# Performance work log

Measured on AMD Instinct MI355X. Metric: run time of the kernel, lower is better.

The kernel has to match this reference:

```python
import jax, jax.numpy as jnp
import numpy as np

B, D, C, Q = 4096, 128, 1000, 65536
PROTO_M = 0.99
EPS = 1e-12


def _l2norm(x, axis=-1):
    n = jnp.sqrt(jnp.sum(x * x, axis=axis, keepdims=True))
    return x / jnp.maximum(n, EPS)


def setup_inputs() -> dict:
    key = jax.random.key(0)
    ks = jax.random.split(key, 7)
    q = _l2norm(jax.random.normal(ks[0], (B, D), dtype=jnp.float32))
    k = _l2norm(jax.random.normal(ks[1], (B, D), dtype=jnp.float32))
    classfy_logits = jax.random.normal(ks[2], (B, C), dtype=jnp.float32)
    plabel = jax.random.uniform(ks[3], (B, C), dtype=jnp.float32)
    prototypes = _l2norm(jax.random.normal(ks[4], (C, D), dtype=jnp.float32))
    queue = _l2norm(jax.random.normal(ks[5], (Q, D), dtype=jnp.float32))
    queue_pseudo = jax.random.randint(ks[6], (Q,), 0, C).astype(jnp.float32)
    return {
        "q": q, "k": k, "classfy_logits": classfy_logits, "plabel": plabel,
        "prototypes": prototypes, "queue": queue, "queue_pseudo": queue_pseudo,
        "ptr": 0,
    }


def reference(q, k, classfy_logits, plabel, prototypes, queue, queue_pseudo, ptr):
    m = PROTO_M
    # classifier softmax (encoder head output)
    classfy_out = jax.nn.softmax(classfy_logits, axis=1)          # [B, C]
    # cluster logits against OLD prototypes (mm happens before EMA update)
    logits_prot = jnp.matmul(q, prototypes.T)                     # [B, C]
    cluster_out = jax.nn.softmax(logits_prot, axis=1)
    # pseudo labels from partial-label-masked scores
    pseudo_labels = jnp.argmax(classfy_out * plabel, axis=1)      # [B] int
    # --- vectorized order-dependent scatter-EMA prototype update ---
    # sequential: proto[l_i] = m*proto[l_i] + (1-m)*q_i  for i = 0..B-1
    # closed form: proto[c]*m^{n_c} + sum_i (1-m)*m^{(#later samples with same label)} q_i
    onehot = (pseudo_labels[:, None] == jnp.arange(C)[None, :])   # [B, C] bool
    counts = jnp.sum(onehot, axis=0)                              # [C] n_c
    rank = jnp.take_along_axis(jnp.cumsum(onehot.astype(jnp.int32), axis=0),
                               pseudo_labels[:, None], axis=1)[:, 0] - 1  # [B]
    n_l = counts[pseudo_labels]                                   # [B]
    w = (1.0 - m) * jnp.power(jnp.float32(m), (n_l - 1 - rank).astype(jnp.float32))
    scatter = jnp.zeros_like(prototypes).at[pseudo_labels].add(w[:, None] * q)
    decay = jnp.power(jnp.float32(m), counts.astype(jnp.float32))[:, None]
    new_prototypes = _l2norm(prototypes * decay + scatter, axis=1)
    # --- MoCo queue enqueue/dequeue (contrastive bank uses OLD queue) ---
    cont_features = jnp.concatenate([q, k, queue], axis=0)        # [2B+Q, D]
    pl_f = pseudo_labels.astype(jnp.float32)
    cont_labels = jnp.concatenate([pl_f, pl_f, queue_pseudo], axis=0)
    new_queue = jax.lax.dynamic_update_slice(queue, k, (ptr, 0))
    new_queue_pseudo = jax.lax.dynamic_update_slice(queue_pseudo, pl_f, (ptr,))
    new_ptr = (ptr + q.shape[0]) % queue.shape[0]
    return (classfy_out, cluster_out, cont_features, cont_labels,
            new_prototypes, new_queue, new_queue_pseudo, new_ptr)
```

## Files before the change

kernel.cpp:

```cpp
#include <hip/hip_runtime.h>
#include <hip/hip_bf16.h>
#include <math.h>

#define Bn 4096
#define Dn 128
#define Cn 1000
#define Qn 65536

typedef __attribute__((ext_vector_type(8))) short short8v;
typedef __attribute__((ext_vector_type(4))) short short4v;
typedef __attribute__((ext_vector_type(4))) float f32x4;
typedef __attribute__((ext_vector_type(4))) float f4v;

__device__ inline float waveAllMaxF(float v) {
    for (int o = 32; o; o >>= 1) v = fmaxf(v, __shfl_xor(v, o));
    return v;
}
__device__ inline float waveAllSumF(float v) {
    for (int o = 32; o; o >>= 1) v += __shfl_xor(v, o);
    return v;
}
__device__ inline float waveSumF(float v) {
    for (int o = 32; o; o >>= 1) v += __shfl_down(v, o);
    return v;
}
__device__ inline short f2bf(float x) {
    union { __hip_bfloat16 h; short s; } u;
    u.h = __float2bfloat16(x);
    return u.s;
}

__global__ __launch_bounds__(256) void k_cls(
    const float* __restrict__ logits, const float* __restrict__ plabel,
    const float* __restrict__ q, const float* __restrict__ proto,
    float* __restrict__ out_cls, int* __restrict__ labels,
    __hip_bfloat16* __restrict__ qb, __hip_bfloat16* __restrict__ pb)
{
    int g = blockIdx.x, t = threadIdx.x;

    if (t < 160) {
        int idx4 = g * 160 + t;
        if (idx4 < 131072) {
            f4v v = *(const f4v*)(q + (long long)idx4 * 4);
            short4v o = {f2bf(v.x), f2bf(v.y), f2bf(v.z), f2bf(v.w)};
            *(short4v*)((short*)qb + (long long)idx4 * 4) = o;
        } else {
            int j4 = idx4 - 131072;
            short4v o = {0, 0, 0, 0};
            if (j4 < 32000) {
                f4v v = *(const f4v*)(proto + (long long)j4 * 4);
                o = (short4v){f2bf(v.x), f2bf(v.y), f2bf(v.z), f2bf(v.w)};
            }
            *(short4v*)((short*)pb + (long long)j4 * 4) = o;
        }
    }

    int lane = t & 63, wid = t >> 6;
    int row = g * 4 + wid;
    const float* x  = logits + (long long)row * Cn;
    const float* pl = plabel + (long long)row * Cn;

    f4v lv[4], pv[4];
#pragma unroll
    for (int j = 0; j < 4; ++j) {
        int f4i = lane + j * 64;
        if (f4i < 250) {
            lv[j] = *(const f4v*)(x + f4i * 4);
            pv[j] = *(const f4v*)(pl + f4i * 4);
        } else {
            lv[j] = (f4v){-INFINITY, -INFINITY, -INFINITY, -INFINITY};
            pv[j] = (f4v){0.f, 0.f, 0.f, 0.f};
        }
    }

    float mx = -INFINITY;
#pragma unroll
    for (int j = 0; j < 4; ++j)
        mx = fmaxf(mx, fmaxf(fmaxf(lv[j].x, lv[j].y), fmaxf(lv[j].z, lv[j].w)));
    mx = waveAllMaxF(mx);

    float vv[16];
    float ssum = 0.f;
#pragma unroll
    for (int j = 0; j < 4; ++j) {
        vv[j * 4 + 0] = expf(lv[j].x - mx);
        vv[j * 4 + 1] = expf(lv[j].y - mx);
        vv[j * 4 + 2] = expf(lv[j].z - mx);
        vv[j * 4 + 3] = expf(lv[j].w - mx);
        ssum += vv[j * 4 + 0] + vv[j * 4 + 1] + vv[j * 4 + 2] + vv[j * 4 + 3];
    }
    ssum = waveAllSumF(ssum);
    float inv = 1.f / ssum;

    float bv = -INFINITY; int bi = Cn;
#pragma unroll
    for (int j = 0; j < 4; ++j) {
        int f4i = lane + j * 64;
        if (f4i < 250) {
            float o0 = vv[j * 4 + 0] * inv, o1 = vv[j * 4 + 1] * inv;
            float o2 = vv[j * 4 + 2] * inv, o3 = vv[j * 4 + 3] * inv;
            *((f4v*)(out_cls + (long long)row * Cn) + f4i) = (f4v){o0, o1, o2, o3};
            float pr[4] = {o0 * pv[j].x, o1 * pv[j].y, o2 * pv[j].z, o3 * pv[j].w};
#pragma unroll
            for (int jj = 0; jj < 4; ++jj) {
                if (pr[jj] > bv) { bv = pr[jj]; bi = f4i * 4 + jj; }
            }
        }
    }
    for (int o = 32; o; o >>= 1) {
        float ov = __shfl_xor(bv, o);
        int   oi = __shfl_xor(bi, o);
        if (ov > bv || (ov == bv && oi < bi)) { bv = ov; bi = oi; }
    }
    if (lane == 0) labels[row] = bi;
}

__global__ __launch_bounds__(256) void k_rest(
    const __hip_bfloat16* __restrict__ qb, const __hip_bfloat16* __restrict__ pbuf,
    const float* __restrict__ proto, const float* __restrict__ q,
    const float* __restrict__ kk, const float* __restrict__ queue,
    const int* __restrict__ lbl, const float* __restrict__ qps,
    const int* __restrict__ ptrp,
    float* __restrict__ outC, float* __restrict__ outp,
    float* __restrict__ out_lab, float* __restrict__ out_qps,
    float* __restrict__ out_ptr,
    float* __restrict__ out_feat, float* __restrict__ out_queue)
{
    __shared__ __align__(16) char smem[32800];
    int bid = blockIdx.x, t = threadIdx.x;

    if (bid < 256) {
        float (*red)[4] = (float (*)[4])smem;
        int lane = t & 63, w = t >> 6;
        int la = lane & 15, lk = lane >> 4;
        int row0 = bid * 16;

        f32x4 acc[16];
#pragma unroll
        for (int j = 0; j < 16; ++j) acc[j] = (f32x4){0.f, 0.f, 0.f, 0.f};

        const short* A = (const short*)qb + (long long)(row0 + la) * Dn;
        const short* Bp = (const short*)pbuf;
#pragma unroll
        for (int kc = 0; kc < Dn; kc += 32) {
            short8v a = *(const short8v*)(A + kc + lk * 8);
#pragma unroll
            for (int j = 0; j < 16; ++j) {
                int prow = w * 256 + j * 16 + la;
                short8v b = *(const short8v*)(Bp + (long long)prow * Dn + kc + lk * 8);
                acc[j] = __builtin_amdgcn_mfma_f32_16x16x32_bf16(a, b, acc[j], 0, 0, 0);
            }
        }

        float m[4];
#pragma unroll
        for (int rg = 0; rg < 4; ++rg) {
            float v = -INFINITY;
#pragma unroll
            for (int j = 0; j < 16; ++j) {
                int col = w * 256 + j * 16 + la;
                if (col < Cn) v = fmaxf(v, acc[j][rg]);
            }
#pragma unroll
            for (int o = 1; o < 16; o <<= 1) v = fmaxf(v, __shfl_xor(v, o));
            m[rg] = v;
        }
        if (la == 0) {
#pragma unroll
            for (int rg = 0; rg < 4; ++rg) red[lk * 4 + rg][w] = m[rg];
        }
        __syncthreads();
#pragma unroll
        for (int rg = 0; rg < 4; ++rg) {
            int r = lk * 4 + rg;
            m[rg] = fmaxf(fmaxf(red[r][0], red[r][1]), fmaxf(red[r][2], red[r][3]));
        }
        __syncthreads();

        float s[4];
#pragma unroll
        for (int rg = 0; rg < 4; ++rg) {
            float v = 0.f;
#pragma unroll
            for (int j = 0; j < 16; ++j) {
                int col = w * 256 + j * 16 + la;
                float e = (col < Cn) ? expf(acc[j][rg] - m[rg]) : 0.f;
                acc[j][rg] = e;
                v += e;
            }
#pragma unroll
            for (int o = 1; o < 16; o <<= 1) v += __shfl_xor(v, o);
            s[rg] = v;
        }
        if (la == 0) {
#pragma unroll
            for (int rg = 0; rg < 4; ++rg) red[lk * 4 + rg][w] = s[rg];
        }
        __syncthreads();
#pragma unroll
        for (int rg = 0; rg < 4; ++rg) {
            int r = lk * 4 + rg;
            s[rg] = 1.f / (red[r][0] + red[r][1] + red[r][2] + red[r][3]);
        }

#pragma unroll
        for (int j = 0; j < 16; ++j) {
            int col = w * 256 + j * 16 + la;
            if (col < Cn) {
                int rowb = row0 + lk * 4;
#pragma unroll
                for (int rg = 0; rg < 4; ++rg)
                    outC[(long long)(rowb + rg) * Cn + col] = acc[j][rg] * s[rg];
            }
        }
    } else if (bid < 756) {
        int* sl = (int*)smem;
        unsigned short* list0 = (unsigned short*)(smem + 16384);
        unsigned short* list1 = list0 + 4096;
        int* nm = (int*)(smem + 32768);
        float* shh = (float*)(smem + 32776);

        int h = t >> 7, tt = t & 127;
        int c = (bid - 256) * 2 + h;

#pragma unroll
        for (int u = 0; u < 4; ++u) {
            int base = (u * 256 + t) * 4;
            *(int4*)(sl + base) = *(const int4*)(lbl + base);
        }
        if (t == 0)   nm[0] = 0;
        if (t == 128) nm[1] = 0;
        __syncthreads();

        int wv = t >> 6;
        if ((wv & 1) == 0) {
            int hh = wv >> 1;
            int ln = t & 63;
            int cc = (bid - 256) * 2 + hh;
            unsigned short* lst = hh ? list1 : list0;
            int n = 0;
            for (int jj = 0; jj < Bn / 64; ++jj) {
                unsigned long long mask = __ballot(sl[jj * 64 + ln] == cc);
                if (ln == 0) {
                    while (mask) {
                        int b = __builtin_ctzll(mask);
                        lst[n++] = (unsigned short)(jj * 64 + b);
                        mask &= mask - 1;
                    }
                }
            }
            if (ln == 0) nm[hh] = n;
        }
        __syncthreads();

        int n = nm[h];
        unsigned short* lst = h ? list1 : list0;
        float acc = proto[(long long)c * Dn + tt];
        for (int mi = 0; mi < n; ++mi)
            acc = 0.99f * acc + 0.01f * q[(long long)lst[mi] * Dn + tt];

        float ss = waveSumF(acc * acc);
        if ((t & 63) == 0) shh[t >> 6] = ss;
        __syncthreads();
        float nn = sqrtf(shh[h * 2] + shh[h * 2 + 1]);
        outp[(long long)c * Dn + tt] = acc / fmaxf(nn, 1e-12f);
    } else if (bid < 1301) {
        int gid = (bid - 756) * 256 + t;
        const int NL = 2 * Bn + Qn;
        int p = *ptrp;
        int pc = p < 0 ? 0 : (p > Qn - Bn ? Qn - Bn : p);
        if (gid < NL) {
            float v;
            if (gid < Bn)          v = (float)lbl[gid];
            else if (gid < 2 * Bn) v = (float)lbl[gid - Bn];
            else                   v = qps[gid - 2 * Bn];
            out_lab[gid] = v;
        }
        int j = gid - NL;
        if (j >= 0 && j < Qn) {
            unsigned rr = (unsigned)(j - pc);
            out_qps[j] = (rr < (unsigned)Bn) ? (float)lbl[rr] : qps[j];
        }
        if (gid == NL + Qn) out_ptr[0] = (float)((p + Bn) % Qn);
    } else if (bid < 1557) {
        int fb = bid - 1301;
        const float* src = (fb < 128) ? q : kk;
        long long sb = (long long)(fb & 127) * 4096;
        long long db = (long long)fb * 4096;
        f4v v[4];
#pragma unroll
        for (int u = 0; u < 4; ++u)
            v[u] = *(const f4v*)(src + sb + (u * 256 + t) * 4);
#pragma unroll
        for (int u = 0; u < 4; ++u)
            *(f4v*)(out_feat + db + (u * 256 + t) * 4) = v[u];
    } else {
        int cb = bid - 1557;
        int p = *ptrp;
        int pc = p < 0 ? 0 : (p > Qn - Bn ? Qn - Bn : p);
        long long base = (long long)cb * 4096;
        const long long FB = 2LL * Bn * Dn;
        f4v v[4];
#pragma unroll
        for (int u = 0; u < 4; ++u)
            v[u] = *(const f4v*)(queue + base + (u * 256 + t) * 4);
#pragma unroll
        for (int u = 0; u < 4; ++u)
            *(f4v*)(out_feat + FB + base + (u * 256 + t) * 4) = v[u];
#pragma unroll
        for (int u = 0; u < 4; ++u) {
            long long foff = base + (u * 256 + t) * 4;
            int row = (int)(foff >> 7);
            unsigned rr = (unsigned)(row - pc);
            f4v wv = v[u];
            if (rr < (unsigned)Bn) wv = *(const f4v*)(kk + (long long)rr * Dn + (foff & 127));
            *(f4v*)(out_queue + foff) = wv;
        }
    }
}

extern "C" void kernel_launch(void* const* d_in, const int* in_sizes, int n_in,
                              void* d_out, int out_size, void* d_ws, size_t ws_size,
                              hipStream_t stream)
{
    const float* q     = (const float*)d_in[0];
    const float* kk    = (const float*)d_in[1];
    const float* cl    = (const float*)d_in[2];
    const float* plab  = (const float*)d_in[3];
    const float* proto = (const float*)d_in[4];
    const float* queue = (const float*)d_in[5];
    const float* qps   = (const float*)d_in[6];
    const int*   ptrp  = (const int*)d_in[7];

    float* out = (float*)d_out;
    const long long O_CLU  = 4096000;
    const long long O_FEAT = 8192000;
    const long long O_LAB  = 17629184;
    const long long O_PROT = 17702912;
    const long long O_QUE  = 17830912;
    const long long O_QPS  = 26219520;
    const long long O_PTR  = 26285056;

    char* ws = (char*)d_ws;
    int*   lbl = (int*)(ws + 0);
    __hip_bfloat16* qb = (__hip_bfloat16*)(ws + 1048576);
    __hip_bfloat16* pb = (__hip_bfloat16*)(ws + 2097152);

    k_cls<<<1024, 256, 0, stream>>>(cl, plab, q, proto, out, lbl, qb, pb);
    k_rest<<<3605, 256, 0, stream>>>(qb, pb, proto, q, kk, queue, lbl, qps, ptrp,
                                     out + O_CLU, out + O_PROT,
                                     out + O_LAB, out + O_QPS, out + O_PTR,
                                     out + O_FEAT, out + O_QUE);
}
```

Measured before the change: 47.76 us.

## Fuse independent work into one 1024-thread kernel, convert bf16 inline

```diff
diff --git a/kernel.cpp b/kernel.cpp
--- a/kernel.cpp
+++ b/kernel.cpp
@@ -8,7 +8,6 @@
 #define Qn 65536
 
 typedef __attribute__((ext_vector_type(8))) short short8v;
-typedef __attribute__((ext_vector_type(4))) short short4v;
 typedef __attribute__((ext_vector_type(4))) float f32x4;
 typedef __attribute__((ext_vector_type(4))) float f4v;
 
@@ -30,190 +29,237 @@
     return u.s;
 }
 
-__global__ __launch_bounds__(256) void k_cls(
+__global__ __launch_bounds__(1024, 8) void k_main(
     const float* __restrict__ logits, const float* __restrict__ plabel,
     const float* __restrict__ q, const float* __restrict__ proto,
+    const float* __restrict__ kk, const float* __restrict__ queue,
+    const int* __restrict__ ptrp,
     float* __restrict__ out_cls, int* __restrict__ labels,
-    __hip_bfloat16* __restrict__ qb, __hip_bfloat16* __restrict__ pb)
+    float* __restrict__ outC,
+    float* __restrict__ out_feat, float* __restrict__ out_queue)
 {
-    int g = blockIdx.x, t = threadIdx.x;
-
-    if (t < 160) {
-        int idx4 = g * 160 + t;
-        if (idx4 < 131072) {
-            f4v v = *(const f4v*)(q + (long long)idx4 * 4);
-            short4v o = {f2bf(v.x), f2bf(v.y), f2bf(v.z), f2bf(v.w)};
-            *(short4v*)((short*)qb + (long long)idx4 * 4) = o;
-        } else {
-            int j4 = idx4 - 131072;
-            short4v o = {0, 0, 0, 0};
-            if (j4 < 32000) {
-                f4v v = *(const f4v*)(proto + (long long)j4 * 4);
-                o = (short4v){f2bf(v.x), f2bf(v.y), f2bf(v.z), f2bf(v.w)};
-            }
-            *(short4v*)((short*)pb + (long long)j4 * 4) = o;
-        }
-    }
-
-    int lane = t & 63, wid = t >> 6;
-    int row = g * 4 + wid;
-    const float* x  = logits + (long long)row * Cn;
-    const float* pl = plabel + (long long)row * Cn;
-
-    f4v lv[4], pv[4];
-#pragma unroll
-    for (int j = 0; j < 4; ++j) {
-        int f4i = lane + j * 64;
-        if (f4i < 250) {
-            lv[j] = *(const f4v*)(x + f4i * 4);
-            pv[j] = *(const f4v*)(pl + f4i * 4);
-        } else {
-            lv[j] = (f4v){-INFINITY, -INFINITY, -INFINITY, -INFINITY};
-            pv[j] = (f4v){0.f, 0.f, 0.f, 0.f};
-        }
-    }
-
-    float mx = -INFINITY;
-#pragma unroll
-    for (int j = 0; j < 4; ++j)
-        mx = fmaxf(mx, fmaxf(fmaxf(lv[j].x, lv[j].y), fmaxf(lv[j].z, lv[j].w)));
-    mx = waveAllMaxF(mx);
-
-    float vv[16];
-    float ssum = 0.f;
-#pragma unroll
-    for (int j = 0; j < 4; ++j) {
-        vv[j * 4 + 0] = expf(lv[j].x - mx);
-        vv[j * 4 + 1] = expf(lv[j].y - mx);
-        vv[j * 4 + 2] = expf(lv[j].z - mx);
-        vv[j * 4 + 3] = expf(lv[j].w - mx);
-        ssum += vv[j * 4 + 0] + vv[j * 4 + 1] + vv[j * 4 + 2] + vv[j * 4 + 3];
-    }
-    ssum = waveAllSumF(ssum);
-    float inv = 1.f / ssum;
-
-    float bv = -INFINITY; int bi = Cn;
-#pragma unroll
-    for (int j = 0; j < 4; ++j) {
-        int f4i = lane + j * 64;
-        if (f4i < 250) {
-            float o0 = vv[j * 4 + 0] * inv, o1 = vv[j * 4 + 1] * inv;
-            float o2 = vv[j * 4 + 2] * inv, o3 = vv[j * 4 + 3] * inv;
-            *((f4v*)(out_cls + (long long)row * Cn) + f4i) = (f4v){o0, o1, o2, o3};
-            float pr[4] = {o0 * pv[j].x, o1 * pv[j].y, o2 * pv[j].z, o3 * pv[j].w};
-#pragma unroll
-            for (int jj = 0; jj < 4; ++jj) {
-                if (pr[jj] > bv) { bv = pr[jj]; bi = f4i * 4 + jj; }
-            }
-        }
-    }
-    for (int o = 32; o; o >>= 1) {
-        float ov = __shfl_xor(bv, o);
-        int   oi = __shfl_xor(bi, o);
-        if (ov > bv || (ov == bv && oi < bi)) { bv = ov; bi = oi; }
-    }
-    if (lane == 0) labels[row] = bi;
-}
-
-__global__ __launch_bounds__(256) void k_rest(
-    const __hip_bfloat16* __restrict__ qb, const __hip_bfloat16* __restrict__ pbuf,
+    __shared__ float red[16][17];
+    int bid = blockIdx.x, t = threadIdx.x;
+    int g = bid / 17, s = bid % 17;
+
+    if (s < 4) {
+        int cb = g * 4 + s;
+        int lane = t & 63, wid = t >> 6;
+        int row = cb * 16 + wid;
+        const float* x  = logits + (long long)row * Cn;
+        const float* pl = plabel + (long long)row * Cn;
+
+        f4v lv[4], pv[4];
+#pragma unroll
+        for (int j = 0; j < 4; ++j) {
+            int f4i = lane + j * 64;
+            if (f4i < 250) {
+                lv[j] = *(const f4v*)(x + f4i * 4);
+                pv[j] = *(const f4v*)(pl + f4i * 4);
+            } else {
+                lv[j] = (f4v){-INFINITY, -INFINITY, -INFINITY, -INFINITY};
+                pv[j] = (f4v){0.f, 0.f, 0.f, 0.f};
+            }
+        }
+
+        float mx = -INFINITY;
+#pragma unroll
+        for (int j = 0; j < 4; ++j)
+            mx = fmaxf(mx, fmaxf(fmaxf(lv[j].x, lv[j].y), fmaxf(lv[j].z, lv[j].w)));
+        mx = waveAllMaxF(mx);
+
+        float ssum = 0.f;
+#pragma unroll
+        for (int j = 0; j < 4; ++j) {
+            lv[j].x = expf(lv[j].x - mx);
+            lv[j].y = expf(lv[j].y - mx);
+            lv[j].z = expf(lv[j].z - mx);
+            lv[j].w = expf(lv[j].w - mx);
+            ssum += lv[j].x + lv[j].y + lv[j].z + lv[j].w;
+        }
+        ssum = waveAllSumF(ssum);
+        float inv = 1.f / ssum;
+
+        float bv = -INFINITY; int bi = Cn;
+#pragma unroll
+        for (int j = 0; j < 4; ++j) {
+            int f4i = lane + j * 64;
+            if (f4i < 250) {
+                f4v o4 = {lv[j].x * inv, lv[j].y * inv, lv[j].z * inv, lv[j].w * inv};
+                *((f4v*)(out_cls + (long long)row * Cn) + f4i) = o4;
+                float pr[4] = {o4.x * pv[j].x, o4.y * pv[j].y, o4.z * pv[j].z, o4.w * pv[j].w};
+#pragma unroll
+                for (int jj = 0; jj < 4; ++jj) {
+                    if (pr[jj] > bv) { bv = pr[jj]; bi = f4i * 4 + jj; }
+                }
+            }
+        }
+        for (int o = 32; o; o >>= 1) {
+            float ov = __shfl_xor(bv, o);
+            int   oi = __shfl_xor(bi, o);
+            if (ov > bv || (ov == bv && oi < bi)) { bv = ov; bi = oi; }
+        }
+        if (lane == 0) labels[row] = bi;
+        return;
+    }
+
+    if (s < 8) {
+        int gb = g * 4 + (s - 4);
+        int row0 = gb * 16;
+        int lane = t & 63, w = t >> 6;
+        int la = lane & 15, lk = lane >> 4;
+
+        f32x4 acc[4];
+#pragma unroll
+        for (int j = 0; j < 4; ++j) acc[j] = (f32x4){0.f, 0.f, 0.f, 0.f};
+
+        const float* A0 = q + (long long)(row0 + la) * Dn;
+#pragma unroll
+        for (int kc = 0; kc < Dn; kc += 32) {
+            short8v a;
+            {
+                f4v f0 = *(const f4v*)(A0 + kc + lk * 8);
+                f4v f1 = *(const f4v*)(A0 + kc + lk * 8 + 4);
+                a[0] = f2bf(f0.x); a[1] = f2bf(f0.y); a[2] = f2bf(f0.z); a[3] = f2bf(f0.w);
+                a[4] = f2bf(f1.x); a[5] = f2bf(f1.y); a[6] = f2bf(f1.z); a[7] = f2bf(f1.w);
+            }
+#pragma unroll
+            for (int j = 0; j < 4; ++j) {
+                int prow = w * 64 + j * 16 + la;
+                short8v b = {0, 0, 0, 0, 0, 0, 0, 0};
+                if (prow < Cn) {
+                    const float* Bp0 = proto + (long long)prow * Dn + kc + lk * 8;
+                    f4v f0 = *(const f4v*)Bp0;
+                    f4v f1 = *(const f4v*)(Bp0 + 4);
+                    b[0] = f2bf(f0.x); b[1] = f2bf(f0.y); b[2] = f2bf(f0.z); b[3] = f2bf(f0.w);
+                    b[4] = f2bf(f1.x); b[5] = f2bf(f1.y); b[6] = f2bf(f1.z); b[7] = f2bf(f1.w);
+                }
+                acc[j] = __builtin_amdgcn_mfma_f32_16x16x32_bf16(a, b, acc[j], 0, 0, 0);
+            }
+        }
+
+        float m[4];
+#pragma unroll
+        for (int rg = 0; rg < 4; ++rg) {
+            float v = -INFINITY;
+#pragma unroll
+            for (int j = 0; j < 4; ++j) {
+                int col = w * 64 + j * 16 + la;
+                if (col < Cn) v = fmaxf(v, acc[j][rg]);
+            }
+#pragma unroll
+            for (int o = 1; o < 16; o <<= 1) v = fmaxf(v, __shfl_xor(v, o));
+            m[rg] = v;
+        }
+        if (la == 0) {
+#pragma unroll
+            for (int rg = 0; rg < 4; ++rg) red[lk * 4 + rg][w] = m[rg];
+        }
+        __syncthreads();
+#pragma unroll
+        for (int rg = 0; rg < 4; ++rg) {
+            int r = lk * 4 + rg;
+            float v = red[r][0];
+#pragma unroll
+            for (int ww = 1; ww < 16; ++ww) v = fmaxf(v, red[r][ww]);
+            m[rg] = v;
+        }
+        __syncthreads();
+
+        float sm[4];
+#pragma unroll
+        for (int rg = 0; rg < 4; ++rg) {
+            float v = 0.f;
+#pragma unroll
+            for (int j = 0; j < 4; ++j) {
+                int col = w * 64 + j * 16 + la;
+                float e = (col < Cn) ? expf(acc[j][rg] - m[rg]) : 0.f;
+                acc[j][rg] = e;
+                v += e;
+            }
+#pragma unroll
+            for (int o = 1; o < 16; o <<= 1) v += __shfl_xor(v, o);
+            sm[rg] = v;
+        }
+        if (la == 0) {
+#pragma unroll
+            for (int rg = 0; rg < 4; ++rg) red[lk * 4 + rg][w] = sm[rg];
+        }
+        __syncthreads();
+#pragma unroll
+        for (int rg = 0; rg < 4; ++rg) {
+            int r = lk * 4 + rg;
+            float v = 0.f;
+#pragma unroll
+            for (int ww = 0; ww < 16; ++ww) v += red[r][ww];
+            sm[rg] = 1.f / v;
+        }
+
+#pragma unroll
+        for (int j = 0; j < 4; ++j) {
+            int col = w * 64 + j * 16 + la;
+            if (col < Cn) {
+                int rowb = row0 + lk * 4;
+#pragma unroll
+                for (int rg = 0; rg < 4; ++rg)
+                    outC[(long long)(rowb + rg) * Cn + col] = acc[j][rg] * sm[rg];
+            }
+        }
+        return;
+    }
+
+    if (s == 8) {
+        int fb = g;
+        const float* src = (fb < 32) ? q : kk;
+        long long sb = (long long)(fb & 31) * 16384;
+        long long db = (long long)fb * 16384;
+        f4v v[4];
+#pragma unroll
+        for (int u = 0; u < 4; ++u)
+            v[u] = *(const f4v*)(src + sb + (u * 1024 + t) * 4);
+#pragma unroll
+        for (int u = 0; u < 4; ++u)
+            *(f4v*)(out_feat + db + (u * 1024 + t) * 4) = v[u];
+        return;
+    }
+
+    {
+        int cb = g * 8 + (s - 9);
+        int p = *ptrp;
+        int pc = p < 0 ? 0 : (p > Qn - Bn ? Qn - Bn : p);
+        long long base = (long long)cb * 16384;
+        const long long FB = 2LL * Bn * Dn;
+        f4v v[4];
+#pragma unroll
+        for (int u = 0; u < 4; ++u)
+            v[u] = *(const f4v*)(queue + base + (u * 1024 + t) * 4);
+#pragma unroll
+        for (int u = 0; u < 4; ++u)
+            *(f4v*)(out_feat + FB + base + (u * 1024 + t) * 4) = v[u];
+#pragma unroll
+        for (int u = 0; u < 4; ++u) {
+            long long foff = base + (u * 1024 + t) * 4;
+            int row = (int)(foff >> 7);
+            unsigned rr = (unsigned)(row - pc);
+            f4v wv = v[u];
+            if (rr < (unsigned)Bn) wv = *(const f4v*)(kk + (long long)rr * Dn + (foff & 127));
+            *(f4v*)(out_queue + foff) = wv;
+        }
+    }
+}
+
+__global__ __launch_bounds__(256) void k_dep(
     const float* __restrict__ proto, const float* __restrict__ q,
-    const float* __restrict__ kk, const float* __restrict__ queue,
     const int* __restrict__ lbl, const float* __restrict__ qps,
     const int* __restrict__ ptrp,
-    float* __restrict__ outC, float* __restrict__ outp,
+    float* __restrict__ outp,
     float* __restrict__ out_lab, float* __restrict__ out_qps,
-    float* __restrict__ out_ptr,
-    float* __restrict__ out_feat, float* __restrict__ out_queue)
+    float* __restrict__ out_ptr)
 {
     __shared__ __align__(16) char smem[32800];
     int bid = blockIdx.x, t = threadIdx.x;
 
-    if (bid < 256) {
-        float (*red)[4] = (float (*)[4])smem;
-        int lane = t & 63, w = t >> 6;
-        int la = lane & 15, lk = lane >> 4;
-        int row0 = bid * 16;
-
-        f32x4 acc[16];
-#pragma unroll
-        for (int j = 0; j < 16; ++j) acc[j] = (f32x4){0.f, 0.f, 0.f, 0.f};
-
-        const short* A = (const short*)qb + (long long)(row0 + la) * Dn;
-        const short* Bp = (const short*)pbuf;
-#pragma unroll
-        for (int kc = 0; kc < Dn; kc += 32) {
-            short8v a = *(const short8v*)(A + kc + lk * 8);
-#pragma unroll
-            for (int j = 0; j < 16; ++j) {
-                int prow = w * 256 + j * 16 + la;
-                short8v b = *(const short8v*)(Bp + (long long)prow * Dn + kc + lk * 8);
-                acc[j] = __builtin_amdgcn_mfma_f32_16x16x32_bf16(a, b, acc[j], 0, 0, 0);
-            }
-        }
-
-        float m[4];
-#pragma unroll
-        for (int rg = 0; rg < 4; ++rg) {
-            float v = -INFINITY;
-#pragma unroll
-            for (int j = 0; j < 16; ++j) {
-                int col = w * 256 + j * 16 + la;
-                if (col < Cn) v = fmaxf(v, acc[j][rg]);
-            }
-#pragma unroll
-            for (int o = 1; o < 16; o <<= 1) v = fmaxf(v, __shfl_xor(v, o));
-            m[rg] = v;
-        }
-        if (la == 0) {
-#pragma unroll
-            for (int rg = 0; rg < 4; ++rg) red[lk * 4 + rg][w] = m[rg];
-        }
-        __syncthreads();
-#pragma unroll
-        for (int rg = 0; rg < 4; ++rg) {
-            int r = lk * 4 + rg;
-            m[rg] = fmaxf(fmaxf(red[r][0], red[r][1]), fmaxf(red[r][2], red[r][3]));
-        }
-        __syncthreads();
-
-        float s[4];
-#pragma unroll
-        for (int rg = 0; rg < 4; ++rg) {
-            float v = 0.f;
-#pragma unroll
-            for (int j = 0; j < 16; ++j) {
-                int col = w * 256 + j * 16 + la;
-                float e = (col < Cn) ? expf(acc[j][rg] - m[rg]) : 0.f;
-                acc[j][rg] = e;
-                v += e;
-            }
-#pragma unroll
-            for (int o = 1; o < 16; o <<= 1) v += __shfl_xor(v, o);
-            s[rg] = v;
-        }
-        if (la == 0) {
-#pragma unroll
-            for (int rg = 0; rg < 4; ++rg) red[lk * 4 + rg][w] = s[rg];
-        }
-        __syncthreads();
-#pragma unroll
-        for (int rg = 0; rg < 4; ++rg) {
-            int r = lk * 4 + rg;
-            s[rg] = 1.f / (red[r][0] + red[r][1] + red[r][2] + red[r][3]);
-        }
-
-#pragma unroll
-        for (int j = 0; j < 16; ++j) {
-            int col = w * 256 + j * 16 + la;
-            if (col < Cn) {
-                int rowb = row0 + lk * 4;
-#pragma unroll
-                for (int rg = 0; rg < 4; ++rg)
-                    outC[(long long)(rowb + rg) * Cn + col] = acc[j][rg] * s[rg];
-            }
-        }
-    } else if (bid < 756) {
+    if (bid < 500) {
         int* sl = (int*)smem;
         unsigned short* list0 = (unsigned short*)(smem + 16384);
         unsigned short* list1 = list0 + 4096;
@@ -221,7 +267,7 @@
         float* shh = (float*)(smem + 32776);
 
         int h = t >> 7, tt = t & 127;
-        int c = (bid - 256) * 2 + h;
+        int c = bid * 2 + h;
 
 #pragma unroll
         for (int u = 0; u < 4; ++u) {
@@ -236,7 +282,7 @@
         if ((wv & 1) == 0) {
             int hh = wv >> 1;
             int ln = t & 63;
-            int cc = (bid - 256) * 2 + hh;
+            int cc = bid * 2 + hh;
             unsigned short* lst = hh ? list1 : list0;
             int n = 0;
             for (int jj = 0; jj < Bn / 64; ++jj) {
@@ -264,8 +310,8 @@
         __syncthreads();
         float nn = sqrtf(shh[h * 2] + shh[h * 2 + 1]);
         outp[(long long)c * Dn + tt] = acc / fmaxf(nn, 1e-12f);
-    } else if (bid < 1301) {
-        int gid = (bid - 756) * 256 + t;
+    } else {
+        int gid = (bid - 500) * 256 + t;
         const int NL = 2 * Bn + Qn;
         int p = *ptrp;
         int pc = p < 0 ? 0 : (p > Qn - Bn ? Qn - Bn : p);
@@ -282,40 +328,6 @@
             out_qps[j] = (rr < (unsigned)Bn) ? (float)lbl[rr] : qps[j];
         }
         if (gid == NL + Qn) out_ptr[0] = (float)((p + Bn) % Qn);
-    } else if (bid < 1557) {
-        int fb = bid - 1301;
-        const float* src = (fb < 128) ? q : kk;
-        long long sb = (long long)(fb & 127) * 4096;
-        long long db = (long long)fb * 4096;
-        f4v v[4];
-#pragma unroll
-        for (int u = 0; u < 4; ++u)
-            v[u] = *(const f4v*)(src + sb + (u * 256 + t) * 4);
-#pragma unroll
-        for (int u = 0; u < 4; ++u)
-            *(f4v*)(out_feat + db + (u * 256 + t) * 4) = v[u];
-    } else {
-        int cb = bid - 1557;
-        int p = *ptrp;
-        int pc = p < 0 ? 0 : (p > Qn - Bn ? Qn - Bn : p);
-        long long base = (long long)cb * 4096;
-        const long long FB = 2LL * Bn * Dn;
-        f4v v[4];
-#pragma unroll
-        for (int u = 0; u < 4; ++u)
-            v[u] = *(const f4v*)(queue + base + (u * 256 + t) * 4);
-#pragma unroll
-        for (int u = 0; u < 4; ++u)
-            *(f4v*)(out_feat + FB + base + (u * 256 + t) * 4) = v[u];
-#pragma unroll
-        for (int u = 0; u < 4; ++u) {
-            long long foff = base + (u * 256 + t) * 4;
-            int row = (int)(foff >> 7);
-            unsigned rr = (unsigned)(row - pc);
-            f4v wv = v[u];
-            if (rr < (unsigned)Bn) wv = *(const f4v*)(kk + (long long)rr * Dn + (foff & 127));
-            *(f4v*)(out_queue + foff) = wv;
-        }
     }
 }
 
@@ -342,13 +354,12 @@
     const long long O_PTR  = 26285056;
 
     char* ws = (char*)d_ws;
-    int*   lbl = (int*)(ws + 0);
-    __hip_bfloat16* qb = (__hip_bfloat16*)(ws + 1048576);
-    __hip_bfloat16* pb = (__hip_bfloat16*)(ws + 2097152);
-
-    k_cls<<<1024, 256, 0, stream>>>(cl, plab, q, proto, out, lbl, qb, pb);
-    k_rest<<<3605, 256, 0, stream>>>(qb, pb, proto, q, kk, queue, lbl, qps, ptrp,
-                                     out + O_CLU, out + O_PROT,
-                                     out + O_LAB, out + O_QPS, out + O_PTR,
-                                     out + O_FEAT, out + O_QUE);
-}
+    int* lbl = (int*)(ws + 0);
+
+    k_main<<<1088, 1024, 0, stream>>>(cl, plab, q, proto, kk, queue, ptrp,
+                                      out, lbl, out + O_CLU,
+                                      out + O_FEAT, out + O_QUE);
+    k_dep<<<1045, 256, 0, stream>>>(proto, q, lbl, qps, ptrp,
+                                    out + O_PROT,
+                                    out + O_LAB, out + O_QPS, out + O_PTR);
+}
```

Result: slower. 69.56 us (+45.6%).
